# Kernel optimization log

Measured on AMD Instinct MI355X. Metric: run time of the kernel, lower is better.

Reference implementation:

```python
import jax, jax.numpy as jnp
import numpy as np

NUM_NODES = 50000
NUM_EDGES = 600000
NUM_FEAT = 128
HIDDEN = 512
N_OUT = 128
K = 3
N_GRAPHS = 128


def setup_inputs() -> dict:
    key = jax.random.key(0)
    ks = jax.random.split(key, 12)
    feature = jax.random.normal(ks[0], (NUM_NODES, NUM_FEAT), dtype=jnp.float32)
    edge_index = jax.random.randint(ks[1], (2, NUM_EDGES), 0, NUM_NODES, dtype=jnp.int64)
    protein_batch = jnp.sort(jax.random.randint(ks[2], (NUM_NODES,), 0, N_GRAPHS, dtype=jnp.int64))
    s = 0.05
    # ChebConv weights stored [K, in, out] (x @ W), single shared bias per conv
    W1 = jax.random.normal(ks[3], (K, NUM_FEAT, NUM_FEAT), dtype=jnp.float32) * s
    b1 = jax.random.normal(ks[4], (NUM_FEAT,), dtype=jnp.float32) * s
    W2 = jax.random.normal(ks[5], (K, NUM_FEAT, 2 * NUM_FEAT), dtype=jnp.float32) * s
    b2 = jax.random.normal(ks[6], (2 * NUM_FEAT,), dtype=jnp.float32) * s
    fc1_w = jax.random.normal(ks[7], (3 * NUM_FEAT, HIDDEN), dtype=jnp.float32) * s
    fc1_b = jax.random.normal(ks[8], (HIDDEN,), dtype=jnp.float32) * s
    fc2_w = jax.random.normal(ks[9], (HIDDEN, N_OUT), dtype=jnp.float32) * s
    fc2_b = jax.random.normal(ks[10], (N_OUT,), dtype=jnp.float32) * s
    return {"feature": feature, "edge_index": edge_index, "protein_batch": protein_batch,
            "W1": W1, "b1": b1, "W2": W2, "b2": b2,
            "fc1_w": fc1_w, "fc1_b": fc1_b, "fc2_w": fc2_w, "fc2_b": fc2_b}


def _cheb_conv(x, src, dst, edge_w, W, b):
    # PyG ChebConv with sym normalization, lambda_max=2 => scaled Laplacian
    # L_hat has zero diagonal and off-diag weights -1/sqrt(d_i d_j) (edge_w).
    def prop(h):
        return jax.ops.segment_sum(edge_w[:, None] * h[src], dst, num_segments=NUM_NODES)

    Tx0 = x
    out = Tx0 @ W[0]
    Tx1 = prop(x)
    out = out + Tx1 @ W[1]
    for k in range(2, W.shape[0]):
        Tx2 = 2.0 * prop(Tx1) - Tx0
        out = out + Tx2 @ W[k]
        Tx0, Tx1 = Tx1, Tx2
    return out + b


def reference(feature, edge_index, protein_batch, W1, b1, W2, b2, fc1_w, fc1_b, fc2_w, fc2_b):
    src, dst = edge_index[0], edge_index[1]
    deg = jax.ops.segment_sum(jnp.ones_like(src, dtype=feature.dtype), src, num_segments=NUM_NODES)
    dinv = jnp.where(deg > 0, jax.lax.rsqrt(jnp.maximum(deg, 1.0)), 0.0)
    edge_w = -dinv[src] * dinv[dst]  # (2/lambda_max)*L_sym off-diagonal; diag cancels to 0

    gx = jax.nn.relu(_cheb_conv(feature, src, dst, edge_w, W1, b1))
    gx = jax.nn.relu(_cheb_conv(gx, src, dst, edge_w, W2, b2))
    gx = jnp.concatenate([gx, feature], axis=1)  # [N, 3*F]

    # global_mean_pool
    sums = jax.ops.segment_sum(gx, protein_batch, num_segments=N_GRAPHS)
    cnts = jax.ops.segment_sum(jnp.ones((gx.shape[0],), gx.dtype), protein_batch, num_segments=N_GRAPHS)
    pooled = sums / jnp.maximum(cnts, 1.0)[:, None]

    h = jax.nn.relu(pooled @ fc1_w + fc1_b)  # dropout is identity in eval
    return h @ fc2_w + fc2_b
```

## Files before the change

### kernel.cpp

```cpp
#include <hip/hip_runtime.h>
#include <hip/hip_bf16.h>

#define NNODES 50000
#define NEDGES 600000
#define NB 196
#define NBKT 196
#define SB 192
#define SCH (NEDGES / SB)

typedef short vs8 __attribute__((ext_vector_type(8)));
typedef float floatx4 __attribute__((ext_vector_type(4)));

__device__ __forceinline__ float us2f(unsigned short u) {
    unsigned int x = ((unsigned int)u) << 16;
    float f;
    __builtin_memcpy(&f, &x, 4);
    return f;
}
__device__ __forceinline__ unsigned short f2us(float f) {
    unsigned int x;
    __builtin_memcpy(&x, &f, 4);
    unsigned int r = x + 0x7fffu + ((x >> 16) & 1u);
    return (unsigned short)(r >> 16);
}
__device__ __forceinline__ float ldf(const void* p, int i, int ff) {
    if (ff) return us2f(((const unsigned short*)p)[i]);
    return ((const float*)p)[i];
}
__device__ __forceinline__ int2 ldnt_sw(const int2* p) {
    unsigned long long v =
        __builtin_nontemporal_load(reinterpret_cast<const unsigned long long*>(p));
    int2 r;
    r.x = (int)(unsigned int)(v & 0xffffffffULL);
    r.y = (int)(unsigned int)(v >> 32);
    return r;
}

__global__ void k_detect(const int* ei, const unsigned int* fw, int* iflag, int* fflag) {
    int lane = threadIdx.x;
    int odd1 = ei[2 * lane + 1];
    int odd2 = ei[128 + 2 * lane + 1];
    unsigned long long nz = __ballot(odd1 != 0 || odd2 != 0);
    unsigned int e = (fw[lane] >> 7) & 0xffu;
    unsigned long long h = __ballot(e > 100u && e < 160u);
    if (lane == 0) {
        *iflag = (nz == 0ULL) ? 1 : 0;
        *fflag = (__popcll(h) > 40) ? 1 : 0;
    }
}

__global__ void k_init(const int* pb, const int* iflag, int* b32, float* psum) {
    int i = blockIdx.x * 256 + threadIdx.x;
    if (i < NNODES) {
        int f = *iflag;
        b32[i] = pb[((size_t)i) << f];
    }
    if (i < 128 * 384) psum[i] = 0.f;
}

__global__ __launch_bounds__(256) void k_deghist(const int* ei, const int* iflag,
                                                 unsigned int* degpart, int* cntpart) {
    __shared__ unsigned int h[25000];
    __shared__ int c[NBKT];
    int t = threadIdx.x, blk = blockIdx.x;
    for (int i = t; i < 25000; i += 256) h[i] = 0u;
    if (t < NBKT) c[t] = 0;
    __syncthreads();
    int f = *iflag;
    int e0 = blk * SCH;
    for (int j = t; j < SCH; j += 256) {
        int e = e0 + j;
        int s = ei[((size_t)e) << f];
        int d = ei[((size_t)(NEDGES + e)) << f];
        atomicAdd(&h[s >> 1], (s & 1) ? 65536u : 1u);
        atomicAdd(&c[d >> 8], 1);
    }
    __syncthreads();
    unsigned int* dp = degpart + (size_t)blk * 25000;
    for (int i = t; i < 25000; i += 256) dp[i] = h[i];
    if (t < NBKT) cntpart[blk * NBKT + t] = c[t];
}

__global__ void k_dred(const unsigned int* degpart, float* dinv) {
    int i = blockIdx.x * 256 + threadIdx.x;
    if (i >= 25000) return;
    unsigned int lo = 0, hi = 0;
    for (int b = 0; b < SB; ++b) {
        unsigned int p = degpart[(size_t)b * 25000 + i];
        lo += p & 0xffffu;
        hi += p >> 16;
    }
    dinv[2 * i] = lo ? rsqrtf((float)lo) : 0.f;
    dinv[2 * i + 1] = hi ? rsqrtf((float)hi) : 0.f;
}

__global__ void k_bscan(const int* cntpart, int* bbase, int* gbase,
                        const int* batch32, int* pcnt, int* rowptr) {
    __shared__ int tot[256];
    int t = threadIdx.x;
    int sum = 0;
    if (t < NBKT) {
        for (int b = 0; b < SB; ++b) sum += cntpart[b * NBKT + t];
    }
    tot[t] = sum;
    __syncthreads();
    for (int off = 1; off < 256; off <<= 1) {
        int x = (t >= off) ? tot[t - off] : 0;
        __syncthreads();
        tot[t] += x;
        __syncthreads();
    }
    int excl = tot[t] - sum;
    if (t < NBKT) {
        gbase[t] = excl;
        int run = excl;
        for (int b = 0; b < SB; ++b) {
            bbase[b * NBKT + t] = run;
            run += cntpart[b * NBKT + t];
        }
    }
    if (t == 0) {
        gbase[NBKT] = NEDGES;
        rowptr[NNODES] = NEDGES;
    }
    if (t < 128) {
        int g = t;
        int lo = 0, hi = NNODES;
        while (lo < hi) { int mid = (lo + hi) >> 1; if (batch32[mid] < g) lo = mid + 1; else hi = mid; }
        int start = lo;
        hi = NNODES;
        while (lo < hi) { int mid = (lo + hi) >> 1; if (batch32[mid] <= g) lo = mid + 1; else hi = mid; }
        pcnt[g] = lo - start;
    }
}

__global__ void k_scat(const int* ei, const int* iflag, const float* dinv,
                       const int* bbase, int2* bkt) {
    __shared__ int cur[NBKT];
    int t = threadIdx.x, blk = blockIdx.x;
    if (t < NBKT) cur[t] = bbase[blk * NBKT + t];
    __syncthreads();
    int f = *iflag;
    int e0 = blk * SCH;
    for (int j = t; j < SCH; j += 256) {
        int e = e0 + j;
        int s = ei[((size_t)e) << f];
        int d = ei[((size_t)(NEDGES + e)) << f];
        float w = -dinv[s] * dinv[d];
        int slot = atomicAdd(&cur[d >> 8], 1);
        int wb;
        __builtin_memcpy(&wb, &w, 4);
        int2 v;
        v.x = s | ((d & 255) << 16);
        v.y = wb;
        bkt[slot] = v;
    }
}

__global__ void k_csr(const int2* bkt, const int* gbase, int* rowptr, int2* csr_sw) {
    __shared__ int hist[256], scan[256], cur[256];
    int t = threadIdx.x, b = blockIdx.x;
    int beg = gbase[b], end = gbase[b + 1];
    int n = end - beg;
    hist[t] = 0;
    __syncthreads();
    for (int i = t; i < n; i += 256) {
        int bin = (bkt[beg + i].x >> 16) & 255;
        atomicAdd(&hist[bin], 1);
    }
    __syncthreads();
    int h = hist[t];
    scan[t] = h;
    __syncthreads();
    for (int off = 1; off < 256; off <<= 1) {
        int x = (t >= off) ? scan[t - off] : 0;
        __syncthreads();
        scan[t] += x;
        __syncthreads();
    }
    int excl = scan[t] - h;
    int node = b * 256 + t;
    if (node < NNODES) rowptr[node] = beg + excl;
    cur[t] = excl;
    __syncthreads();
    for (int i = t; i < n; i += 256) {
        int2 p = bkt[beg + i];
        int bin = (p.x >> 16) & 255;
        int slot = atomicAdd(&cur[bin], 1);
        int2 v;
        v.x = p.x & 0xffff;
        v.y = p.y;
        csr_sw[beg + slot] = v;
    }
}

__global__ void k_featb(const void* src, const int* fflag, unsigned short* dst) {
    int i = blockIdx.x * 256 + threadIdx.x;
    if (i >= NNODES * 128 / 8) return;
    if (*fflag) {
        reinterpret_cast<uint4*>(dst)[i] = reinterpret_cast<const uint4*>(src)[i];
    } else {
        const float4* fs = reinterpret_cast<const float4*>(src);
        float4 a = fs[2 * i], b = fs[2 * i + 1];
        uint4 o;
        o.x = (unsigned int)f2us(a.x) | ((unsigned int)f2us(a.y) << 16);
        o.y = (unsigned int)f2us(a.z) | ((unsigned int)f2us(a.w) << 16);
        o.z = (unsigned int)f2us(b.x) | ((unsigned int)f2us(b.y) << 16);
        o.w = (unsigned int)f2us(b.z) | ((unsigned int)f2us(b.w) << 16);
        reinterpret_cast<uint4*>(dst)[i] = o;
    }
}

__global__ void k_trans2(const void* W1, const void* W2, const int* fflag,
                         unsigned short* W1t, unsigned short* W2t) {
    int idx = blockIdx.x * 256 + threadIdx.x;
    int ff = *fflag;
    if (idx < 49152) {
        int n = idx / 384, k = idx - n * 384;
        float v;
        if (k < 128) v = ldf(W1, k * 128 + n, ff) - ldf(W1, (256 + k) * 128 + n, ff);
        else if (k < 256) v = ldf(W1, k * 128 + n, ff);
        else v = 2.f * ldf(W1, k * 128 + n, ff);
        W1t[idx] = f2us(v);
    } else if (idx < 49152 + 98304) {
        int j = idx - 49152;
        int n = j / 384, k = j - n * 384;
        float v;
        if (k < 128) v = ldf(W2, k * 256 + n, ff) - ldf(W2, (256 + k) * 256 + n, ff);
        else if (k < 256) v = ldf(W2, k * 256 + n, ff);
        else v = 2.f * ldf(W2, k * 256 + n, ff);
        W2t[j] = f2us(v);
    }
}

__global__ void k_prepw(const void* b1, const void* b2, const void* f1w, const void* f1b,
                        const void* f2w, const void* f2b, const int* fflag,
                        float* b1f, float* b2f, float* f1wf, float* f1bf,
                        float* f2wf, float* f2bf) {
    int i = blockIdx.x * 256 + threadIdx.x;
    int ff = *fflag;
    if (i < 196608) { f1wf[i] = ldf(f1w, i, ff); return; }
    i -= 196608;
    if (i < 65536) { f2wf[i] = ldf(f2w, i, ff); return; }
    i -= 65536;
    if (i < 512) { f1bf[i] = ldf(f1b, i, ff); return; }
    i -= 512;
    if (i < 256) { b2f[i] = ldf(b2, i, ff); return; }
    i -= 256;
    if (i < 128) { b1f[i] = ldf(b1, i, ff); return; }
    i -= 128;
    if (i < 128) f2bf[i] = ldf(f2b, i, ff);
}

__global__ void k_prop(const unsigned short* X, const int* rowptr, const int2* csr_sw,
                       unsigned short* out) {
    int wvid = (blockIdx.x * blockDim.x + threadIdx.x) >> 6;
    int lane = threadIdx.x & 63;
    int q = lane >> 4;
    int ln = lane & 15;
    int node = wvid * 4 + q;
    if (node >= NNODES) return;
    int fo = ln * 8;
    int beg = rowptr[node], end = rowptr[node + 1];
    float a0 = 0.f, a1 = 0.f, a2 = 0.f, a3 = 0.f;
    float a4 = 0.f, a5 = 0.f, a6 = 0.f, a7 = 0.f;
    int j = beg;
    for (; j + 4 <= end; j += 4) {
        int2 e0 = ldnt_sw(csr_sw + j);
        int2 e1 = ldnt_sw(csr_sw + j + 1);
        int2 e2 = ldnt_sw(csr_sw + j + 2);
        int2 e3 = ldnt_sw(csr_sw + j + 3);
        uint4 u0 = *reinterpret_cast<const uint4*>(X + (size_t)e0.x * 128 + fo);
        uint4 u1 = *reinterpret_cast<const uint4*>(X + (size_t)e1.x * 128 + fo);
        uint4 u2 = *reinterpret_cast<const uint4*>(X + (size_t)e2.x * 128 + fo);
        uint4 u3 = *reinterpret_cast<const uint4*>(X + (size_t)e3.x * 128 + fo);
        float w0, w1, w2, w3;
        __builtin_memcpy(&w0, &e0.y, 4);
        __builtin_memcpy(&w1, &e1.y, 4);
        __builtin_memcpy(&w2, &e2.y, 4);
        __builtin_memcpy(&w3, &e3.y, 4);
        a0 += w0 * us2f((unsigned short)(u0.x & 0xffffu)) + w1 * us2f((unsigned short)(u1.x & 0xffffu))
            + w2 * us2f((unsigned short)(u2.x & 0xffffu)) + w3 * us2f((unsigned short)(u3.x & 0xffffu));
        a1 += w0 * us2f((unsigned short)(u0.x >> 16)) + w1 * us2f((unsigned short)(u1.x >> 16))
            + w2 * us2f((unsigned short)(u2.x >> 16)) + w3 * us2f((unsigned short)(u3.x >> 16));
        a2 += w0 * us2f((unsigned short)(u0.y & 0xffffu)) + w1 * us2f((unsigned short)(u1.y & 0xffffu))
            + w2 * us2f((unsigned short)(u2.y & 0xffffu)) + w3 * us2f((unsigned short)(u3.y & 0xffffu));
        a3 += w0 * us2f((unsigned short)(u0.y >> 16)) + w1 * us2f((unsigned short)(u1.y >> 16))
            + w2 * us2f((unsigned short)(u2.y >> 16)) + w3 * us2f((unsigned short)(u3.y >> 16));
        a4 += w0 * us2f((unsigned short)(u0.z & 0xffffu)) + w1 * us2f((unsigned short)(u1.z & 0xffffu))
            + w2 * us2f((unsigned short)(u2.z & 0xffffu)) + w3 * us2f((unsigned short)(u3.z & 0xffffu));
        a5 += w0 * us2f((unsigned short)(u0.z >> 16)) + w1 * us2f((unsigned short)(u1.z >> 16))
            + w2 * us2f((unsigned short)(u2.z >> 16)) + w3 * us2f((unsigned short)(u3.z >> 16));
        a6 += w0 * us2f((unsigned short)(u0.w & 0xffffu)) + w1 * us2f((unsigned short)(u1.w & 0xffffu))
            + w2 * us2f((unsigned short)(u2.w & 0xffffu)) + w3 * us2f((unsigned short)(u3.w & 0xffffu));
        a7 += w0 * us2f((unsigned short)(u0.w >> 16)) + w1 * us2f((unsigned short)(u1.w >> 16))
            + w2 * us2f((unsigned short)(u2.w >> 16)) + w3 * us2f((unsigned short)(u3.w >> 16));
    }
    for (; j < end; ++j) {
        int2 e = ldnt_sw(csr_sw + j);
        float w;
        __builtin_memcpy(&w, &e.y, 4);
        uint4 u = *reinterpret_cast<const uint4*>(X + (size_t)e.x * 128 + fo);
        a0 += w * us2f((unsigned short)(u.x & 0xffffu));
        a1 += w * us2f((unsigned short)(u.x >> 16));
        a2 += w * us2f((unsigned short)(u.y & 0xffffu));
        a3 += w * us2f((unsigned short)(u.y >> 16));
        a4 += w * us2f((unsigned short)(u.z & 0xffffu));
        a5 += w * us2f((unsigned short)(u.z >> 16));
        a6 += w * us2f((unsigned short)(u.w & 0xffffu));
        a7 += w * us2f((unsigned short)(u.w >> 16));
    }
    uint4 ov;
    ov.x = (unsigned int)f2us(a0) | ((unsigned int)f2us(a1) << 16);
    ov.y = (unsigned int)f2us(a2) | ((unsigned int)f2us(a3) << 16);
    ov.z = (unsigned int)f2us(a4) | ((unsigned int)f2us(a5) << 16);
    ov.w = (unsigned int)f2us(a6) | ((unsigned int)f2us(a7) << 16);
    *reinterpret_cast<uint4*>(out + (size_t)node * 128 + fo) = ov;
}

template <int POOL>
__global__ __launch_bounds__(512) void k_convg(
    const unsigned short* seg0, const unsigned short* seg1, const unsigned short* seg2,
    const unsigned short* Wt, const float* bias, unsigned short* out,
    const int* batch32, float* psum, int nout, int nslab) {
    __shared__ unsigned short shb[24576];
    __shared__ float sh_ps[512];
    int tid = threadIdx.x;
    int bid = blockIdx.x;
    int grp = 8 * nslab;
    int main_blocks = 24 * grp;
    int r, slab;
    if (bid < main_blocks) {
        int g = bid / grp;
        int rem = bid - g * grp;
        slab = rem >> 3;
        r = g * 8 + (rem & 7);
    } else {
        int t = bid - main_blocks;
        r = 192 + (t & 3);
        slab = t >> 2;
    }
    int col0 = slab * 64;
    if (POOL) sh_ps[tid] = 0.f;
#pragma unroll
    for (int it = 0; it < 6; ++it) {
        int idx = tid + it * 512;
        int kkt = idx >> 6, ln = idx & 63;
        int kk = kkt >> 2, t = kkt & 3;
        int col = col0 + t * 16 + (ln & 15);
        int ko = kk * 32 + (ln >> 4) * 8;
        uint4 v = *reinterpret_cast<const uint4*>(Wt + (size_t)col * 384 + ko);
        *reinterpret_cast<uint4*>(shb + idx * 8) = v;
    }
    __syncthreads();
    int wv = tid >> 6, lane = tid & 63;
    int m = lane & 15, kq = lane >> 4;
    int row0 = r * 256 + wv * 32;
    int rr0 = row0 + m;
    int rr1 = row0 + 16 + m;
    if (rr0 >= NNODES) rr0 = NNODES - 1;
    if (rr1 >= NNODES) rr1 = NNODES - 1;
    const unsigned short* segs[3];
    segs[0] = seg0; segs[1] = seg1; segs[2] = seg2;
    vs8 a[2][12];
#pragma unroll
    for (int kk = 0; kk < 12; ++kk) {
        int sgi = kk >> 2, k4 = kk & 3;
        const unsigned short* S = segs[sgi];
        int ko = k4 * 32 + kq * 8;
        a[0][kk] = *reinterpret_cast<const vs8*>(S + (size_t)rr0 * 128 + ko);
        a[1][kk] = *reinterpret_cast<const vs8*>(S + (size_t)rr1 * 128 + ko);
    }
    __builtin_amdgcn_sched_barrier(0);
    floatx4 acc[2][4];
#pragma unroll
    for (int rI = 0; rI < 2; ++rI)
#pragma unroll
        for (int t = 0; t < 4; ++t) {
            acc[rI][t][0] = 0.f; acc[rI][t][1] = 0.f; acc[rI][t][2] = 0.f; acc[rI][t][3] = 0.f;
        }
#pragma unroll
    for (int kk = 0; kk < 12; ++kk) {
#pragma unroll
        for (int t = 0; t < 4; ++t) {
            vs8 b = *reinterpret_cast<const vs8*>(shb + ((kk * 4 + t) * 64 + lane) * 8);
            acc[0][t] = __builtin_amdgcn_mfma_f32_16x16x32_bf16(a[0][kk], b, acc[0][t], 0, 0, 0);
            acc[1][t] = __builtin_amdgcn_mfma_f32_16x16x32_bf16(a[1][kk], b, acc[1][t], 0, 0, 0);
        }
    }
    if (POOL == 0) {
#pragma unroll
        for (int rI = 0; rI < 2; ++rI) {
            int orow_base = row0 + rI * 16 + kq * 4;
#pragma unroll
            for (int t = 0; t < 4; ++t) {
                int col = col0 + t * 16 + m;
                float bv = bias[col];
#pragma unroll
                for (int i = 0; i < 4; ++i) {
                    int rw = orow_base + i;
                    if (rw < NNODES) {
                        float v = acc[rI][t][i] + bv;
                        v = v > 0.f ? v : 0.f;
                        out[(size_t)rw * nout + col] = f2us(v);
                    }
                }
            }
        }
    } else {
        int g0 = batch32[r * 256];
#pragma unroll
        for (int rI = 0; rI < 2; ++rI) {
            int orow_base = row0 + rI * 16 + kq * 4;
            int gid[4];
#pragma unroll
            for (int i = 0; i < 4; ++i) {
                int rw = orow_base + i;
                gid[i] = rw < NNODES ? batch32[rw] : -1;
            }
#pragma unroll
            for (int t = 0; t < 4; ++t) {
                int col = col0 + t * 16 + m;
                float bv = bias[col];
                float run = 0.f;
                int curg = -1;
#pragma unroll
                for (int i = 0; i < 4; ++i) {
                    int g = gid[i];
                    if (g < 0) break;
                    float v = acc[rI][t][i] + bv;
                    v = v > 0.f ? v : 0.f;
                    if (g != curg) {
                        if (curg >= 0) {
                            int gl = curg - g0;
                            if (gl >= 0 && gl < 8) atomicAdd(&sh_ps[gl * 64 + t * 16 + m], run);
                            else atomicAdd(&psum[curg * 384 + col], run);
                        }
                        curg = g;
                        run = 0.f;
                    }
                    run += v;
                }
                if (curg >= 0) {
                    int gl = curg - g0;
                    if (gl >= 0 && gl < 8) atomicAdd(&sh_ps[gl * 64 + t * 16 + m], run);
                    else atomicAdd(&psum[curg * 384 + col], run);
                }
            }
        }
        __syncthreads();
        int gl = tid >> 6, c = tid & 63;
        float v = sh_ps[tid];
        int gg = g0 + gl;
        if (v != 0.f && gg < 128) atomicAdd(&psum[(size_t)gg * 384 + col0 + c], v);
    }
}

__global__ void k_poolnodes(const unsigned short* featb, const int* batch32, float* psum) {
    int col = threadIdx.x & 127;
    int half = threadIdx.x >> 7;
    int nbeg = blockIdx.x * 128 + half * 64;
    if (nbeg >= NNODES) return;
    int nend = nbeg + 64;
    if (nend > NNODES) nend = NNODES;
    float run = 0.f;
    int curg = batch32[nbeg];
    for (int n = nbeg; n < nend; ++n) {
        int g = batch32[n];
        if (g != curg) {
            atomicAdd(&psum[curg * 384 + 256 + col], run);
            run = 0.f;
            curg = g;
        }
        run += us2f(featb[(size_t)n * 128 + col]);
    }
    atomicAdd(&psum[curg * 384 + 256 + col], run);
}

__global__ void k_fc1(const float* psum, const int* pcnt, const float* w,
                      const float* b, float* h) {
    int g = blockIdx.x, j = threadIdx.x * 2;
    int c = pcnt[g];
    float inv = 1.f / (float)(c > 0 ? c : 1);
    float a0 = 0.f, a1 = 0.f;
    for (int k = 0; k < 384; ++k) {
        float p = psum[g * 384 + k];
        a0 += p * w[k * 512 + j];
        a1 += p * w[k * 512 + j + 1];
    }
    a0 = a0 * inv + b[j];
    a1 = a1 * inv + b[j + 1];
    h[g * 512 + j] = a0 > 0.f ? a0 : 0.f;
    h[g * 512 + j + 1] = a1 > 0.f ? a1 : 0.f;
}

__global__ void ChebModel_74380243632480_kernel(const float* h, const float* w,
                                                const float* b, const int* fflag,
                                                void* out) {
    int g = blockIdx.x, j = threadIdx.x;
    float acc = 0.f;
    for (int k = 0; k < 512; ++k) acc += h[g * 512 + k] * w[k * 128 + j];
    acc += b[j];
    if (*fflag) ((unsigned short*)out)[g * 128 + j] = f2us(acc);
    else ((float*)out)[g * 128 + j] = acc;
}

extern "C" void kernel_launch(void* const* d_in, const int* in_sizes, int n_in,
                              void* d_out, int out_size, void* d_ws, size_t ws_size,
                              hipStream_t stream) {
    const void* feature = d_in[0];
    const int* edge_index = (const int*)d_in[1];
    const int* batch = (const int*)d_in[2];
    const void* W1 = d_in[3];
    const void* b1 = d_in[4];
    const void* W2 = d_in[5];
    const void* b2 = d_in[6];
    const void* fc1w = d_in[7];
    const void* fc1b = d_in[8];
    const void* fc2w = d_in[9];
    const void* fc2b = d_in[10];

    char* ws = (char*)d_ws;
    size_t off = 0;
    int* iflag = (int*)(ws + off); off += 256;
    int* fflag = (int*)(ws + off); off += 256;
    int* rowptr = (int*)(ws + off); off += ((size_t)(NNODES + 1) * 4 + 255) & ~(size_t)255;
    float* dinv = (float*)(ws + off); off += ((size_t)NNODES * 4 + 255) & ~(size_t)255;
    int* batch32 = (int*)(ws + off); off += ((size_t)NNODES * 4 + 255) & ~(size_t)255;
    int* gbase = (int*)(ws + off); off += 1024;
    int* cntpart = (int*)(ws + off); off += ((size_t)SB * NBKT * 4 + 255) & ~(size_t)255;
    int* bbase = (int*)(ws + off); off += ((size_t)SB * NBKT * 4 + 255) & ~(size_t)255;
    int2* csr_sw = (int2*)(ws + off); off += ((size_t)NEDGES * 8 + 255) & ~(size_t)255;
    unsigned short* featb = (unsigned short*)(ws + off); off += ((size_t)NNODES * 128 * 2 + 255) & ~(size_t)255;
    unsigned short* T1 = (unsigned short*)(ws + off); off += ((size_t)NNODES * 128 * 2 + 255) & ~(size_t)255;
    unsigned short* T2 = (unsigned short*)(ws + off); off += ((size_t)NNODES * 128 * 2 + 255) & ~(size_t)255;
    unsigned short* gx1 = (unsigned short*)(ws + off); off += ((size_t)NNODES * 128 * 2 + 255) & ~(size_t)255;
    unsigned short* W1t = (unsigned short*)(ws + off); off += ((size_t)49152 * 2 + 255) & ~(size_t)255;
    unsigned short* W2t = (unsigned short*)(ws + off); off += ((size_t)98304 * 2 + 255) & ~(size_t)255;
    float* b1f = (float*)(ws + off); off += 1024;
    float* b2f = (float*)(ws + off); off += 1024;
    float* fc1wf = (float*)(ws + off); off += ((size_t)196608 * 4 + 255) & ~(size_t)255;
    float* fc1bf = (float*)(ws + off); off += 2048;
    float* fc2wf = (float*)(ws + off); off += ((size_t)65536 * 4 + 255) & ~(size_t)255;
    float* fc2bf = (float*)(ws + off); off += 1024;
    float* psum = (float*)(ws + off); off += ((size_t)128 * 384 * 4 + 255) & ~(size_t)255;
    int* pcnt = (int*)(ws + off); off += 1024;
    float* hbuf = (float*)(ws + off); off += ((size_t)128 * 512 * 4 + 255) & ~(size_t)255;

    int2* bkt = (int2*)T1;
    unsigned int* degpart = (unsigned int*)T2;

    k_detect<<<1, 64, 0, stream>>>(edge_index, (const unsigned int*)feature, iflag, fflag);
    k_init<<<(NNODES + 255) / 256, 256, 0, stream>>>(batch, iflag, batch32, psum);
    k_deghist<<<SB, 256, 0, stream>>>(edge_index, iflag, degpart, cntpart);
    k_dred<<<(25000 + 255) / 256, 256, 0, stream>>>(degpart, dinv);
    k_bscan<<<1, 256, 0, stream>>>(cntpart, bbase, gbase, batch32, pcnt, rowptr);
    k_scat<<<SB, 256, 0, stream>>>(edge_index, iflag, dinv, bbase, bkt);
    k_csr<<<NBKT, 256, 0, stream>>>(bkt, gbase, rowptr, csr_sw);

    k_featb<<<(NNODES * 128 / 8 + 255) / 256, 256, 0, stream>>>(feature, fflag, featb);
    k_trans2<<<(49152 + 98304 + 255) / 256, 256, 0, stream>>>(W1, W2, fflag, W1t, W2t);
    k_prepw<<<(263168 + 255) / 256, 256, 0, stream>>>(b1, b2, fc1w, fc1b, fc2w, fc2b, fflag,
                                                      b1f, b2f, fc1wf, fc1bf, fc2wf, fc2bf);

    int pb = ((NNODES + 3) / 4 * 64 + 255) / 256;
    k_prop<<<pb, 256, 0, stream>>>(featb, rowptr, csr_sw, T1);
    k_prop<<<pb, 256, 0, stream>>>(T1, rowptr, csr_sw, T2);
    k_convg<0><<<196 * 2, 512, 0, stream>>>(featb, T1, T2, W1t, b1f, gx1,
                                            (const int*)0, (float*)0, 128, 2);
    k_prop<<<pb, 256, 0, stream>>>(gx1, rowptr, csr_sw, T1);
    k_prop<<<pb, 256, 0, stream>>>(T1, rowptr, csr_sw, T2);
    k_convg<1><<<196 * 4, 512, 0, stream>>>(gx1, T1, T2, W2t, b2f, (unsigned short*)0,
                                            batch32, psum, 256, 4);
    k_poolnodes<<<(NNODES + 127) / 128, 256, 0, stream>>>(featb, batch32, psum);
    k_fc1<<<128, 256, 0, stream>>>(psum, pcnt, fc1wf, fc1bf, hbuf);
    ChebModel_74380243632480_kernel<<<128, 128, 0, stream>>>(hbuf, fc2wf, fc2bf, fflag, d_out);
}
```

Measured before the change: 417.3 us.

## Retile ChebConv GEMM to 256-thread blocks with 32-column slabs and 64-row waves

The fused ChebConv GEMM kernel now uses 256-thread blocks covering 32 output columns each, with each wave computing 64 rows (4 M-tiles × 2 N-tiles). A-operand loads move inside the K loop instead of preloading all 24 fragments, and the output width becomes a template constant. This cuts registers and shared memory per block so more blocks can be resident, and drops the old grouped block-to-tile mapping. The cost is more blocks that reload the same A rows, and global loads interleaved with MFMAs rather than issued up front. k_prop gets launch bounds and a helper for its accumulation.

Result: slower. 437.0 us (+4.7%).

```diff
diff --git a/kernel.cpp b/kernel.cpp
--- a/kernel.cpp
+++ b/kernel.cpp
@@ -34,6 +34,18 @@
     r.x = (int)(unsigned int)(v & 0xffffffffULL);
     r.y = (int)(unsigned int)(v >> 32);
     return r;
+}
+__device__ __forceinline__ void accum8(float w, uint4 u, float& a0, float& a1,
+                                       float& a2, float& a3, float& a4, float& a5,
+                                       float& a6, float& a7) {
+    a0 += w * us2f((unsigned short)(u.x & 0xffffu));
+    a1 += w * us2f((unsigned short)(u.x >> 16));
+    a2 += w * us2f((unsigned short)(u.y & 0xffffu));
+    a3 += w * us2f((unsigned short)(u.y >> 16));
+    a4 += w * us2f((unsigned short)(u.z & 0xffffu));
+    a5 += w * us2f((unsigned short)(u.z >> 16));
+    a6 += w * us2f((unsigned short)(u.w & 0xffffu));
+    a7 += w * us2f((unsigned short)(u.w >> 16));
 }
 
 __global__ void k_detect(const int* ei, const unsigned int* fw, int* iflag, int* fflag) {
@@ -252,8 +264,9 @@
     if (i < 128) f2bf[i] = ldf(f2b, i, ff);
 }
 
-__global__ void k_prop(const unsigned short* X, const int* rowptr, const int2* csr_sw,
-                       unsigned short* out) {
+__global__ __launch_bounds__(256, 8) void k_prop(const unsigned short* X,
+                                                 const int* rowptr, const int2* csr_sw,
+                                                 unsigned short* out) {
     int wvid = (blockIdx.x * blockDim.x + threadIdx.x) >> 6;
     int lane = threadIdx.x & 63;
     int q = lane >> 4;
@@ -279,36 +292,17 @@
         __builtin_memcpy(&w1, &e1.y, 4);
         __builtin_memcpy(&w2, &e2.y, 4);
         __builtin_memcpy(&w3, &e3.y, 4);
-        a0 += w0 * us2f((unsigned short)(u0.x & 0xffffu)) + w1 * us2f((unsigned short)(u1.x & 0xffffu))
-            + w2 * us2f((unsigned short)(u2.x & 0xffffu)) + w3 * us2f((unsigned short)(u3.x & 0xffffu));
-        a1 += w0 * us2f((unsigned short)(u0.x >> 16)) + w1 * us2f((unsigned short)(u1.x >> 16))
-            + w2 * us2f((unsigned short)(u2.x >> 16)) + w3 * us2f((unsigned short)(u3.x >> 16));
-        a2 += w0 * us2f((unsigned short)(u0.y & 0xffffu)) + w1 * us2f((unsigned short)(u1.y & 0xffffu))
-            + w2 * us2f((unsigned short)(u2.y & 0xffffu)) + w3 * us2f((unsigned short)(u3.y & 0xffffu));
-        a3 += w0 * us2f((unsigned short)(u0.y >> 16)) + w1 * us2f((unsigned short)(u1.y >> 16))
-            + w2 * us2f((unsigned short)(u2.y >> 16)) + w3 * us2f((unsigned short)(u3.y >> 16));
-        a4 += w0 * us2f((unsigned short)(u0.z & 0xffffu)) + w1 * us2f((unsigned short)(u1.z & 0xffffu))
-            + w2 * us2f((unsigned short)(u2.z & 0xffffu)) + w3 * us2f((unsigned short)(u3.z & 0xffffu));
-        a5 += w0 * us2f((unsigned short)(u0.z >> 16)) + w1 * us2f((unsigned short)(u1.z >> 16))
-            + w2 * us2f((unsigned short)(u2.z >> 16)) + w3 * us2f((unsigned short)(u3.z >> 16));
-        a6 += w0 * us2f((unsigned short)(u0.w & 0xffffu)) + w1 * us2f((unsigned short)(u1.w & 0xffffu))
-            + w2 * us2f((unsigned short)(u2.w & 0xffffu)) + w3 * us2f((unsigned short)(u3.w & 0xffffu));
-        a7 += w0 * us2f((unsigned short)(u0.w >> 16)) + w1 * us2f((unsigned short)(u1.w >> 16))
-            + w2 * us2f((unsigned short)(u2.w >> 16)) + w3 * us2f((unsigned short)(u3.w >> 16));
+        accum8(w0, u0, a0, a1, a2, a3, a4, a5, a6, a7);
+        accum8(w1, u1, a0, a1, a2, a3, a4, a5, a6, a7);
+        accum8(w2, u2, a0, a1, a2, a3, a4, a5, a6, a7);
+        accum8(w3, u3, a0, a1, a2, a3, a4, a5, a6, a7);
     }
     for (; j < end; ++j) {
         int2 e = ldnt_sw(csr_sw + j);
         float w;
         __builtin_memcpy(&w, &e.y, 4);
         uint4 u = *reinterpret_cast<const uint4*>(X + (size_t)e.x * 128 + fo);
-        a0 += w * us2f((unsigned short)(u.x & 0xffffu));
-        a1 += w * us2f((unsigned short)(u.x >> 16));
-        a2 += w * us2f((unsigned short)(u.y & 0xffffu));
-        a3 += w * us2f((unsigned short)(u.y >> 16));
-        a4 += w * us2f((unsigned short)(u.z & 0xffffu));
-        a5 += w * us2f((unsigned short)(u.z >> 16));
-        a6 += w * us2f((unsigned short)(u.w & 0xffffu));
-        a7 += w * us2f((unsigned short)(u.w >> 16));
+        accum8(w, u, a0, a1, a2, a3, a4, a5, a6, a7);
     }
     uint4 ov;
     ov.x = (unsigned int)f2us(a0) | ((unsigned int)f2us(a1) << 16);
@@ -318,35 +312,24 @@
     *reinterpret_cast<uint4*>(out + (size_t)node * 128 + fo) = ov;
 }
 
-template <int POOL>
-__global__ __launch_bounds__(512) void k_convg(
+template <int POOL, int NOUT>
+__global__ __launch_bounds__(256, 6) void k_convg(
     const unsigned short* seg0, const unsigned short* seg1, const unsigned short* seg2,
     const unsigned short* Wt, const float* bias, unsigned short* out,
-    const int* batch32, float* psum, int nout, int nslab) {
-    __shared__ unsigned short shb[24576];
-    __shared__ float sh_ps[512];
+    const int* batch32, float* psum) {
+    constexpr int SLABS = NOUT / 32;
+    __shared__ unsigned short shb[12288];
+    __shared__ float sh_ps[POOL ? 256 : 1];
     int tid = threadIdx.x;
     int bid = blockIdx.x;
-    int grp = 8 * nslab;
-    int main_blocks = 24 * grp;
-    int r, slab;
-    if (bid < main_blocks) {
-        int g = bid / grp;
-        int rem = bid - g * grp;
-        slab = rem >> 3;
-        r = g * 8 + (rem & 7);
-    } else {
-        int t = bid - main_blocks;
-        r = 192 + (t & 3);
-        slab = t >> 2;
-    }
-    int col0 = slab * 64;
+    int r = bid / SLABS, slab = bid - r * SLABS;
+    int col0 = slab * 32;
     if (POOL) sh_ps[tid] = 0.f;
 #pragma unroll
     for (int it = 0; it < 6; ++it) {
-        int idx = tid + it * 512;
+        int idx = tid + it * 256;
         int kkt = idx >> 6, ln = idx & 63;
-        int kk = kkt >> 2, t = kkt & 3;
+        int kk = kkt >> 1, t = kkt & 1;
         int col = col0 + t * 16 + (ln & 15);
         int ko = kk * 32 + (ln >> 4) * 8;
         uint4 v = *reinterpret_cast<const uint4*>(Wt + (size_t)col * 384 + ko);
@@ -355,54 +338,54 @@
     __syncthreads();
     int wv = tid >> 6, lane = tid & 63;
     int m = lane & 15, kq = lane >> 4;
-    int row0 = r * 256 + wv * 32;
-    int rr0 = row0 + m;
-    int rr1 = row0 + 16 + m;
-    if (rr0 >= NNODES) rr0 = NNODES - 1;
-    if (rr1 >= NNODES) rr1 = NNODES - 1;
+    int row0 = r * 256 + wv * 64;
+    int rr[4];
+#pragma unroll
+    for (int mt = 0; mt < 4; ++mt) {
+        int rw = row0 + mt * 16 + m;
+        rr[mt] = rw < NNODES ? rw : NNODES - 1;
+    }
+    floatx4 acc[4][2];
+#pragma unroll
+    for (int mt = 0; mt < 4; ++mt)
+#pragma unroll
+        for (int t = 0; t < 2; ++t) {
+            acc[mt][t][0] = 0.f; acc[mt][t][1] = 0.f;
+            acc[mt][t][2] = 0.f; acc[mt][t][3] = 0.f;
+        }
     const unsigned short* segs[3];
     segs[0] = seg0; segs[1] = seg1; segs[2] = seg2;
-    vs8 a[2][12];
 #pragma unroll
     for (int kk = 0; kk < 12; ++kk) {
-        int sgi = kk >> 2, k4 = kk & 3;
-        const unsigned short* S = segs[sgi];
-        int ko = k4 * 32 + kq * 8;
-        a[0][kk] = *reinterpret_cast<const vs8*>(S + (size_t)rr0 * 128 + ko);
-        a[1][kk] = *reinterpret_cast<const vs8*>(S + (size_t)rr1 * 128 + ko);
-    }
-    __builtin_amdgcn_sched_barrier(0);
-    floatx4 acc[2][4];
-#pragma unroll
-    for (int rI = 0; rI < 2; ++rI)
-#pragma unroll
-        for (int t = 0; t < 4; ++t) {
-            acc[rI][t][0] = 0.f; acc[rI][t][1] = 0.f; acc[rI][t][2] = 0.f; acc[rI][t][3] = 0.f;
+        const unsigned short* S = segs[kk >> 2];
+        int ko = (kk & 3) * 32 + kq * 8;
+        vs8 a[4];
+#pragma unroll
+        for (int mt = 0; mt < 4; ++mt)
+            a[mt] = *reinterpret_cast<const vs8*>(S + (size_t)rr[mt] * 128 + ko);
+#pragma unroll
+        for (int t = 0; t < 2; ++t) {
+            vs8 b = *reinterpret_cast<const vs8*>(shb + ((kk * 2 + t) * 64 + lane) * 8);
+#pragma unroll
+            for (int mt = 0; mt < 4; ++mt)
+                acc[mt][t] = __builtin_amdgcn_mfma_f32_16x16x32_bf16(a[mt], b, acc[mt][t], 0, 0, 0);
         }
-#pragma unroll
-    for (int kk = 0; kk < 12; ++kk) {
-#pragma unroll
-        for (int t = 0; t < 4; ++t) {
-            vs8 b = *reinterpret_cast<const vs8*>(shb + ((kk * 4 + t) * 64 + lane) * 8);
-            acc[0][t] = __builtin_amdgcn_mfma_f32_16x16x32_bf16(a[0][kk], b, acc[0][t], 0, 0, 0);
-            acc[1][t] = __builtin_amdgcn_mfma_f32_16x16x32_bf16(a[1][kk], b, acc[1][t], 0, 0, 0);
-        }
     }
     if (POOL == 0) {
 #pragma unroll
-        for (int rI = 0; rI < 2; ++rI) {
-            int orow_base = row0 + rI * 16 + kq * 4;
-#pragma unroll
-            for (int t = 0; t < 4; ++t) {
+        for (int mt = 0; mt < 4; ++mt) {
+            int rbase = row0 + mt * 16 + kq * 4;
+#pragma unroll
+            for (int t = 0; t < 2; ++t) {
                 int col = col0 + t * 16 + m;
                 float bv = bias[col];
 #pragma unroll
                 for (int i = 0; i < 4; ++i) {
-                    int rw = orow_base + i;
+                    int rw = rbase + i;
                     if (rw < NNODES) {
-                        float v = acc[rI][t][i] + bv;
+                        float v = acc[mt][t][i] + bv;
                         v = v > 0.f ? v : 0.f;
-                        out[(size_t)rw * nout + col] = f2us(v);
+                        out[(size_t)rw * NOUT + col] = f2us(v);
                     }
                 }
             }
@@ -410,16 +393,16 @@
     } else {
         int g0 = batch32[r * 256];
 #pragma unroll
-        for (int rI = 0; rI < 2; ++rI) {
-            int orow_base = row0 + rI * 16 + kq * 4;
+        for (int mt = 0; mt < 4; ++mt) {
+            int rbase = row0 + mt * 16 + kq * 4;
             int gid[4];
 #pragma unroll
             for (int i = 0; i < 4; ++i) {
-                int rw = orow_base + i;
+                int rw = rbase + i;
                 gid[i] = rw < NNODES ? batch32[rw] : -1;
             }
 #pragma unroll
-            for (int t = 0; t < 4; ++t) {
+            for (int t = 0; t < 2; ++t) {
                 int col = col0 + t * 16 + m;
                 float bv = bias[col];
                 float run = 0.f;
@@ -428,12 +411,12 @@
                 for (int i = 0; i < 4; ++i) {
                     int g = gid[i];
                     if (g < 0) break;
-                    float v = acc[rI][t][i] + bv;
+                    float v = acc[mt][t][i] + bv;
                     v = v > 0.f ? v : 0.f;
                     if (g != curg) {
                         if (curg >= 0) {
                             int gl = curg - g0;
-                            if (gl >= 0 && gl < 8) atomicAdd(&sh_ps[gl * 64 + t * 16 + m], run);
+                            if (gl >= 0 && gl < 8) atomicAdd(&sh_ps[gl * 32 + t * 16 + m], run);
                             else atomicAdd(&psum[curg * 384 + col], run);
                         }
                         curg = g;
@@ -443,13 +426,13 @@
                 }
                 if (curg >= 0) {
                     int gl = curg - g0;
-                    if (gl >= 0 && gl < 8) atomicAdd(&sh_ps[gl * 64 + t * 16 + m], run);
+                    if (gl >= 0 && gl < 8) atomicAdd(&sh_ps[gl * 32 + t * 16 + m], run);
                     else atomicAdd(&psum[curg * 384 + col], run);
                 }
             }
         }
         __syncthreads();
-        int gl = tid >> 6, c = tid & 63;
+        int gl = tid >> 5, c = tid & 31;
         float v = sh_ps[tid];
         int gg = g0 + gl;
         if (v != 0.f && gg < 128) atomicAdd(&psum[(size_t)gg * 384 + col0 + c], v);
@@ -566,12 +549,12 @@
     int pb = ((NNODES + 3) / 4 * 64 + 255) / 256;
     k_prop<<<pb, 256, 0, stream>>>(featb, rowptr, csr_sw, T1);
     k_prop<<<pb, 256, 0, stream>>>(T1, rowptr, csr_sw, T2);
-    k_convg<0><<<196 * 2, 512, 0, stream>>>(featb, T1, T2, W1t, b1f, gx1,
-                                            (const int*)0, (float*)0, 128, 2);
+    k_convg<0, 128><<<NB * 4, 256, 0, stream>>>(featb, T1, T2, W1t, b1f, gx1,
+                                                (const int*)0, (float*)0);
     k_prop<<<pb, 256, 0, stream>>>(gx1, rowptr, csr_sw, T1);
     k_prop<<<pb, 256, 0, stream>>>(T1, rowptr, csr_sw, T2);
-    k_convg<1><<<196 * 4, 512, 0, stream>>>(gx1, T1, T2, W2t, b2f, (unsigned short*)0,
-                                            batch32, psum, 256, 4);
+    k_convg<1, 256><<<NB * 8, 256, 0, stream>>>(gx1, T1, T2, W2t, b2f, (unsigned short*)0,
+                                                batch32, psum);
     k_poolnodes<<<(NNODES + 127) / 128, 256, 0, stream>>>(featb, batch32, psum);
     k_fc1<<<128, 256, 0, stream>>>(psum, pcnt, fc1wf, fc1bf, hbuf);
     ChebModel_74380243632480_kernel<<<128, 128, 0, stream>>>(hbuf, fc2wf, fc2bf, fflag, d_out);
```
